# Performance work log

Measured on AMD Instinct MI355X. Metric: run time of the kernel, lower is better.

The kernel has to match this reference:

```python
import jax, jax.numpy as jnp
import numpy as np


def _lstm_layer(x, w_ih, w_hh, b_ih, b_hh):
    # x: [B,T,I]; w_ih: [4H,I]; w_hh: [4H,H]. PyTorch gate order: i,f,g,o.
    B, T, _ = x.shape
    H = w_hh.shape[1]
    xg = jnp.einsum('bti,gi->btg', x, w_ih) + b_ih  # precompute input gates [B,T,4H]

    def step(carry, xt):
        h, c = carry
        g = xt + h @ w_hh.T + b_hh
        i, f, gg, o = jnp.split(g, 4, axis=-1)
        c = jax.nn.sigmoid(f) * c + jax.nn.sigmoid(i) * jnp.tanh(gg)
        h = jax.nn.sigmoid(o) * jnp.tanh(c)
        return (h, c), h

    init = (jnp.zeros((B, H), x.dtype), jnp.zeros((B, H), x.dtype))
    _, hs = jax.lax.scan(step, init, jnp.swapaxes(xg, 0, 1))  # [T,B,H]
    return jnp.swapaxes(hs, 0, 1)


def _lstm2(x, p):  # 2-layer stacked LSTM; p = list of 2 layer param tuples
    for (wih, whh, bih, bhh) in p:
        x = _lstm_layer(x, wih, whh, bih, bhh)
    return x


def setup_inputs() -> dict:
    key = jax.random.key(0)
    ks = iter(jax.random.split(key, 32))
    d = {'x': jax.random.normal(next(ks), (100, 75, 75), jnp.float32)}
    specs = {
        'w_ih_1_0': (512, 75), 'w_hh_1_0': (512, 128), 'b_ih_1_0': (512,), 'b_hh_1_0': (512,),
        'w_ih_1_1': (512, 128), 'w_hh_1_1': (512, 128), 'b_ih_1_1': (512,), 'b_hh_1_1': (512,),
        'w_ih_2_0': (256, 128), 'w_hh_2_0': (256, 64), 'b_ih_2_0': (256,), 'b_hh_2_0': (256,),
        'w_ih_2_1': (256, 64), 'w_hh_2_1': (256, 64), 'b_ih_2_1': (256,), 'b_hh_2_1': (256,),
        'w_ih_3_0': (128, 64), 'w_hh_3_0': (128, 32), 'b_ih_3_0': (128,), 'b_hh_3_0': (128,),
        'w_ih_3_1': (128, 32), 'w_hh_3_1': (128, 32), 'b_ih_3_1': (128,), 'b_hh_3_1': (128,),
        'lin_w': (60, 2400), 'lin_b': (60,),
    }
    for name, shp in specs.items():
        d[name] = jax.random.normal(next(ks), shp, jnp.float32) * 0.1
    return d


def reference(x,
              w_ih_1_0, w_hh_1_0, b_ih_1_0, b_hh_1_0,
              w_ih_1_1, w_hh_1_1, b_ih_1_1, b_hh_1_1,
              w_ih_2_0, w_hh_2_0, b_ih_2_0, b_hh_2_0,
              w_ih_2_1, w_hh_2_1, b_ih_2_1, b_hh_2_1,
              w_ih_3_0, w_hh_3_0, b_ih_3_0, b_hh_3_0,
              w_ih_3_1, w_hh_3_1, b_ih_3_1, b_hh_3_1,
              lin_w, lin_b):
    x = _lstm2(x, [(w_ih_1_0, w_hh_1_0, b_ih_1_0, b_hh_1_0),
                   (w_ih_1_1, w_hh_1_1, b_ih_1_1, b_hh_1_1)])
    x = _lstm2(x, [(w_ih_2_0, w_hh_2_0, b_ih_2_0, b_hh_2_0),
                   (w_ih_2_1, w_hh_2_1, b_ih_2_1, b_hh_2_1)])
    x = _lstm2(x, [(w_ih_3_0, w_hh_3_0, b_ih_3_0, b_hh_3_0),
                   (w_ih_3_1, w_hh_3_1, b_ih_3_1, b_hh_3_1)])
    x = x.reshape((100, 32 * 75))  # [B, T*H] (row-major, matches torch)
    return x @ lin_w.T + lin_b
```

## Files before the change

kernel.cpp:

```cpp
#include <hip/hip_runtime.h>

using half8 = __attribute__((ext_vector_type(8))) _Float16;
using f32x4 = __attribute__((ext_vector_type(4))) float;

__device__ __forceinline__ float sigmf(float x) {
    return __builtin_amdgcn_rcpf(1.0f + __expf(-x));
}
__device__ __forceinline__ float tanhx(float x) {
    return 1.0f - 2.0f * __builtin_amdgcn_rcpf(1.0f + __expf(x + x));
}

struct PrepPtrs {
    const float* wih[6];
    const float* whh[6];
    const float* bi[6];
    const float* bh[6];
    const float* lw;
    _Float16* wihI0;
    _Float16* wihI1;
    _Float16* wihI2;
    _Float16* wihP3;
    _Float16* wihP4;
    _Float16* wihP5;
    _Float16* whhP[6];
    float* biasI;
    float* biasP;
    _Float16* lwI;
};

__global__ __launch_bounds__(256) void prep_kernel(PrepPtrs p) {
    int i = blockIdx.x * 256 + threadIdx.x;
    if (i < 38912) {
        int n = i / 76, k = i - n * 76;
        int col = n >> 2, G = n & 3;
        float v = (k < 75) ? p.wih[0][(size_t)(G * 128 + col) * 75 + k] : 0.0f;
        p.wihI0[i] = (_Float16)v;
        return;
    }
    i -= 38912;
    if (i < 65536) {
        int n = i >> 7, k = i & 127;
        int col = n >> 2, G = n & 3;
        p.wihI1[i] = (_Float16)p.wih[1][(size_t)(G * 128 + col) * 128 + k];
        return;
    }
    i -= 65536;
    if (i < 32768) {
        int n = i >> 7, k = i & 127;
        int col = n >> 2, G = n & 3;
        p.wihI2[i] = (_Float16)p.wih[2][(size_t)(G * 64 + col) * 128 + k];
        return;
    }
    i -= 32768;
    if (i < 16384) { p.wihP3[i] = (_Float16)p.wih[3][i]; return; }
    i -= 16384;
    if (i < 8192) { p.wihP4[i] = (_Float16)p.wih[4][i]; return; }
    i -= 8192;
    if (i < 4096) { p.wihP5[i] = (_Float16)p.wih[5][i]; return; }
    i -= 4096;
    constexpr int WHHC[6] = {65536, 65536, 16384, 16384, 4096, 4096};
    #pragma unroll
    for (int l = 0; l < 6; ++l) {
        if (i < WHHC[l]) { p.whhP[l][i] = (_Float16)p.whh[l][i]; return; }
        i -= WHHC[l];
    }
    if (i < 153600) {
        int t = i >> 11;
        int rem = i & 2047;
        int tile = rem >> 9, op = (rem >> 5) & 15, hc = rem & 31;
        int o = tile * 16 + op;
        float v = (o < 60) ? p.lw[(size_t)o * 2400 + t * 32 + hc] : 0.0f;
        p.lwI[i] = (_Float16)v;
        return;
    }
    i -= 153600;
    constexpr int BIH[3] = {128, 128, 64};
    constexpr int BIO[3] = {0, 512, 1024};
    #pragma unroll
    for (int j = 0; j < 3; ++j) {
        int cnt = 4 * BIH[j];
        if (i < cnt) {
            int col = i >> 2, G = i & 3;
            int src = G * BIH[j] + col;
            p.biasI[BIO[j] + i] = p.bi[j][src] + p.bh[j][src];
            return;
        }
        i -= cnt;
    }
    if (i < 256) { p.biasP[i] = p.bi[3][i] + p.bh[3][i]; return; }
    i -= 256;
    if (i < 128) { p.biasP[256 + i] = p.bi[4][i] + p.bh[4][i]; return; }
    i -= 128;
    if (i < 128) { p.biasP[384 + i] = p.bi[5][i] + p.bh[5][i]; return; }
}

__global__ __launch_bounds__(256) void gemm_xg0(
    const float* __restrict__ X,
    const _Float16* __restrict__ W,
    const float* __restrict__ bias, float* __restrict__ C) {
    constexpr int Ks = 3, KP = 96, LDK = 104, HP = 48, Kv = 76, N = 512;
    __shared__ __align__(16) _Float16 Al[64][LDK];
    __shared__ __align__(16) _Float16 Wl[64][LDK];

    const int tid = threadIdx.x;
    const int tt = blockIdx.x >> 1;
    const int boff = (blockIdx.x & 1) * 48;
    const int n0 = blockIdx.y * 64;

    for (int idx = tid; idx < 64 * HP; idx += 256) {
        int row = idx / HP;
        int k = (idx - row * HP) * 2;
        unsigned int va = 0, vw = 0;
        int b = boff + row;
        if (b < 100 && k < 75) {
            float f0 = X[((size_t)b * 75 + tt) * 75 + k];
            float f1 = (k + 1 < 75) ? X[((size_t)b * 75 + tt) * 75 + k + 1] : 0.0f;
            _Float16 h2[2] = {(_Float16)f0, (_Float16)f1};
            va = *(unsigned int*)h2;
        }
        if (k < Kv) vw = *(const unsigned int*)(W + (size_t)(n0 + row) * Kv + k);
        *(unsigned int*)&Al[row][k] = va;
        *(unsigned int*)&Wl[row][k] = vw;
    }
    __syncthreads();

    const int w = tid >> 6, l = tid & 63, hi = l >> 4;
    half8 a[Ks];
    #pragma unroll
    for (int kk = 0; kk < Ks; ++kk)
        a[kk] = *(const half8*)&Al[w * 16 + (l & 15)][kk * 32 + hi * 8];

    f32x4 acc[4];
    #pragma unroll
    for (int jt = 0; jt < 4; ++jt) {
        acc[jt] = f32x4{0.f, 0.f, 0.f, 0.f};
        #pragma unroll
        for (int kk = 0; kk < Ks; ++kk) {
            half8 b = *(const half8*)&Wl[jt * 16 + (l & 15)][kk * 32 + hi * 8];
            acc[jt] = __builtin_amdgcn_mfma_f32_16x16x32_f16(a[kk], b, acc[jt], 0, 0, 0);
        }
    }

    const int bx = (boff >> 2) + w * 4 + hi;
    #pragma unroll
    for (int jt = 0; jt < 4; ++jt) {
        int n = n0 + jt * 16 + (l & 15);
        float bs = bias[n];
        f32x4 v = acc[jt];
        v[0] += bs; v[1] += bs; v[2] += bs; v[3] += bs;
        *(f32x4*)(C + ((size_t)(tt * 28 + bx) * N + n) * 4) = v;
    }
}

template <int Ks>
__global__ __launch_bounds__(256) void gemm_xg(
    const _Float16* __restrict__ A, const _Float16* __restrict__ W,
    const float* __restrict__ bias, float* __restrict__ C, int Kv, int N) {
    constexpr int KP = Ks * 32;
    constexpr int LDK = KP + 8;
    __shared__ __align__(16) _Float16 Al[64][LDK];
    __shared__ __align__(16) _Float16 Wl[64][LDK];

    const int tid = threadIdx.x;
    const int tt = blockIdx.x >> 1;
    const int boff = (blockIdx.x & 1) * 48;
    const int n0 = blockIdx.y * 64;
    constexpr int HP = KP / 2;

    for (int idx = tid; idx < 64 * HP; idx += 256) {
        int row = idx / HP;
        int k = (idx - row * HP) * 2;
        unsigned int va = 0, vw = 0;
        if (k < Kv) {
            va = *(const unsigned int*)(A + (size_t)(tt * 112 + boff + row) * Kv + k);
            vw = *(const unsigned int*)(W + (size_t)(n0 + row) * Kv + k);
        }
        *(unsigned int*)&Al[row][k] = va;
        *(unsigned int*)&Wl[row][k] = vw;
    }
    __syncthreads();

    const int w = tid >> 6, l = tid & 63, hi = l >> 4;
    half8 a[Ks];
    #pragma unroll
    for (int kk = 0; kk < Ks; ++kk)
        a[kk] = *(const half8*)&Al[w * 16 + (l & 15)][kk * 32 + hi * 8];

    f32x4 acc[4];
    #pragma unroll
    for (int jt = 0; jt < 4; ++jt) {
        acc[jt] = f32x4{0.f, 0.f, 0.f, 0.f};
        #pragma unroll
        for (int kk = 0; kk < Ks; ++kk) {
            half8 b = *(const half8*)&Wl[jt * 16 + (l & 15)][kk * 32 + hi * 8];
            acc[jt] = __builtin_amdgcn_mfma_f32_16x16x32_f16(a[kk], b, acc[jt], 0, 0, 0);
        }
    }

    const int bx = (boff >> 2) + w * 4 + hi;
    #pragma unroll
    for (int jt = 0; jt < 4; ++jt) {
        int n = n0 + jt * 16 + (l & 15);
        float bs = bias[n];
        f32x4 v = acc[jt];
        v[0] += bs; v[1] += bs; v[2] += bs; v[3] += bs;
        *(f32x4*)(C + ((size_t)(tt * 28 + bx) * N + n) * 4) = v;
    }
}

#define FTAIL                                                                 \
    __builtin_amdgcn_sched_barrier(0);                                        \
    asm volatile("s_waitcnt lgkmcnt(0)");                                     \
    __builtin_amdgcn_sched_barrier(0);                                        \
    __builtin_amdgcn_s_barrier();                                             \
    __builtin_amdgcn_sched_barrier(0);

#define PICK(A4) ((hi & 2) ? ((hi & 1) ? A4[3] : A4[2]) : ((hi & 1) ? A4[1] : A4[0]))

#define ACT(aI, aF, aG4, aO)                                                  \
    float gI = PICK(aI), gF = PICK(aF), gG = PICK(aG4), gO = PICK(aO);        \
    float si = sigmf(gI), sf = sigmf(gF), tg = tanhx(gG), so = sigmf(gO);     \
    float cn = sf * cst + si * tg;                                            \
    cst = cn;                                                                 \
    float hn = so * tanhx(cn);                                                \
    _Float16 hv = (_Float16)hn;

template <int H>
__global__ __launch_bounds__(4 * H) void lstm_rec(
    const float* __restrict__ xg, const _Float16* __restrict__ whh,
    _Float16* __restrict__ hout) {
    constexpr int Ks = H / 32;
    constexpr int LDH = H + 8;
    constexpr int XSTR = 448 * H;
    constexpr int HSTR = 112 * H;

    __shared__ __align__(16) _Float16 hbuf[2][4][LDH];

    const int tid = threadIdx.x;
    const int w = tid >> 6, l = tid & 63, hi = l >> 4;
    const int col = w * 16 + (l & 15);
    const int blk = blockIdx.x;

    half8 bw[4][Ks];
    #pragma unroll
    for (int G = 0; G < 4; ++G)
        #pragma unroll
        for (int kk = 0; kk < Ks; ++kk)
            bw[G][kk] = *(const half8*)(whh + (size_t)(G * H + col) * H + kk * 32 + hi * 8);

    for (int i = tid; i < 2 * 4 * LDH; i += 4 * H) ((_Float16*)hbuf)[i] = (_Float16)0;
    __syncthreads();

    const float* xp = xg + (size_t)blk * (4 * H * 4) + col * 16;
    _Float16* hop = hout + (size_t)(blk * 4 + hi) * H + col;

    f32x4 P0[4], P1[4], P2[4];
#define XLOAD(PA)                                                             \
    PA[0] = *(const f32x4*)(xp + 0);                                          \
    PA[1] = *(const f32x4*)(xp + 4);                                          \
    PA[2] = *(const f32x4*)(xp + 8);                                          \
    PA[3] = *(const f32x4*)(xp + 12);                                         \
    xp += XSTR;

    XLOAD(P0)
    XLOAD(P1)
    XLOAD(P2)

    float cst = 0.f;

#define LSTM_STEP(PA, CUR)                                                    \
    {                                                                         \
        half8 afr[Ks];                                                        \
        _Pragma("unroll") for (int kk = 0; kk < Ks; ++kk)                     \
            afr[kk] = *(const half8*)&hbuf[CUR][(l & 15) & 3][kk * 32 + hi * 8]; \
        f32x4 aI = PA[0], aF = PA[1], aG4 = PA[2], aO = PA[3];                \
        XLOAD(PA)                                                             \
        _Pragma("unroll") for (int kk = 0; kk < Ks; ++kk) {                   \
            aI = __builtin_amdgcn_mfma_f32_16x16x32_f16(afr[kk], bw[0][kk], aI, 0, 0, 0);  \
            aF = __builtin_amdgcn_mfma_f32_16x16x32_f16(afr[kk], bw[1][kk], aF, 0, 0, 0);  \
            aG4 = __builtin_amdgcn_mfma_f32_16x16x32_f16(afr[kk], bw[2][kk], aG4, 0, 0, 0);\
            aO = __builtin_amdgcn_mfma_f32_16x16x32_f16(afr[kk], bw[3][kk], aO, 0, 0, 0);  \
        }                                                                     \
        ACT(aI, aF, aG4, aO)                                                  \
        hbuf[CUR ^ 1][hi][col] = hv;                                          \
        *hop = hv;                                                            \
        hop += HSTR;                                                          \
        FTAIL                                                                 \
    }

    #pragma unroll 1
    for (int it = 0; it < 12; ++it) {
        LSTM_STEP(P0, 0) LSTM_STEP(P1, 1) LSTM_STEP(P2, 0)
        LSTM_STEP(P0, 1) LSTM_STEP(P1, 0) LSTM_STEP(P2, 1)
    }
    LSTM_STEP(P0, 0) LSTM_STEP(P1, 1) LSTM_STEP(P2, 0)
#undef LSTM_STEP
#undef XLOAD
}

__global__ __launch_bounds__(832) void lstm_quad(
    const float* __restrict__ xg,
    const _Float16* __restrict__ whh2, const _Float16* __restrict__ whh3,
    const _Float16* __restrict__ wih3, const _Float16* __restrict__ whh4,
    const _Float16* __restrict__ wih4, const _Float16* __restrict__ whh5,
    const _Float16* __restrict__ wih5, const float* __restrict__ biasP,
    const _Float16* __restrict__ lwI,
    const float* __restrict__ lb,
    float* __restrict__ outF) {
    __shared__ __align__(16) _Float16 hb2[2][4][72], hp2[2][4][72];
    __shared__ __align__(16) _Float16 hb3[2][4][72], hp3[2][4][72];
    __shared__ __align__(16) _Float16 hb4[2][4][40], hp4[2][4][40];
    __shared__ __align__(16) _Float16 hb5[2][4][40];

    const int tid = threadIdx.x;
    const int w = tid >> 6, l = tid & 63, hi = l >> 4;
    const int lr = (l & 15) & 3;
    const int blk = blockIdx.x;

    for (int i = tid; i < 2 * 4 * 72; i += 832) {
        ((_Float16*)hb2)[i] = (_Float16)0; ((_Float16*)hp2)[i] = (_Float16)0;
        ((_Float16*)hb3)[i] = (_Float16)0; ((_Float16*)hp3)[i] = (_Float16)0;
    }
    for (int i = tid; i < 2 * 4 * 40; i += 832) {
        ((_Float16*)hb4)[i] = (_Float16)0; ((_Float16*)hp4)[i] = (_Float16)0;
        ((_Float16*)hb5)[i] = (_Float16)0;
    }
    __syncthreads();

    float cst = 0.f;

    if (w < 4) {
        const int col = w * 16 + (l & 15);
        half8 bw[4][2];
        #pragma unroll
        for (int G = 0; G < 4; ++G)
            #pragma unroll
            for (int kk = 0; kk < 2; ++kk)
                bw[G][kk] = *(const half8*)(whh2 + (size_t)(G * 64 + col) * 64 + kk * 32 + hi * 8);
        const float* xp = xg + (size_t)blk * 1024 + col * 16;
        f32x4 P0[4], P1[4], P2[4];
#define XLOADQ(PA)                                                            \
        PA[0] = *(const f32x4*)(xp + 0);                                      \
        PA[1] = *(const f32x4*)(xp + 4);                                      \
        PA[2] = *(const f32x4*)(xp + 8);                                      \
        PA[3] = *(const f32x4*)(xp + 12);                                     \
        xp += 28672;
        XLOADQ(P0)
        XLOADQ(P1)
        XLOADQ(P2)

#define QA(PA, CUR, S)                                                        \
        {                                                                     \
            if ((S) < 75) {                                                   \
                half8 afr[2];                                                 \
                _Pragma("unroll") for (int kk = 0; kk < 2; ++kk)              \
                    afr[kk] = *(const half8*)&hb2[CUR][lr][kk * 32 + hi * 8]; \
                f32x4 aI = PA[0], aF = PA[1], aG4 = PA[2], aO = PA[3];        \
                XLOADQ(PA)                                                    \
                _Pragma("unroll") for (int kk = 0; kk < 2; ++kk) {            \
                    aI = __builtin_amdgcn_mfma_f32_16x16x32_f16(afr[kk], bw[0][kk], aI, 0, 0, 0);  \
                    aF = __builtin_amdgcn_mfma_f32_16x16x32_f16(afr[kk], bw[1][kk], aF, 0, 0, 0);  \
                    aG4 = __builtin_amdgcn_mfma_f32_16x16x32_f16(afr[kk], bw[2][kk], aG4, 0, 0, 0);\
                    aO = __builtin_amdgcn_mfma_f32_16x16x32_f16(afr[kk], bw[3][kk], aO, 0, 0, 0);  \
                }                                                             \
                ACT(aI, aF, aG4, aO)                                          \
                hb2[(CUR) ^ 1][hi][col] = hv;                                 \
                hp2[(CUR) ^ 1][hi][col] = hv;                                 \
            }                                                                 \
            FTAIL                                                             \
        }
        #pragma unroll 1
        for (int it = 0; it < 13; ++it) {
            const int b6 = it * 6;
            QA(P0, 0, b6 + 0) QA(P1, 1, b6 + 1) QA(P2, 0, b6 + 2)
            QA(P0, 1, b6 + 3) QA(P1, 0, b6 + 4) QA(P2, 1, b6 + 5)
        }
#undef QA
#undef XLOADQ
    } else if (w < 8) {
        const int col = (w - 4) * 16 + (l & 15);
        half8 bwB[4][2], bwI[4][2];
        #pragma unroll
        for (int G = 0; G < 4; ++G)
            #pragma unroll
            for (int kk = 0; kk < 2; ++kk) {
                bwB[G][kk] = *(const half8*)(whh3 + (size_t)(G * 64 + col) * 64 + kk * 32 + hi * 8);
                bwI[G][kk] = *(const half8*)(wih3 + (size_t)(G * 64 + col) * 64 + kk * 32 + hi * 8);
            }
        const float bI = biasP[col], bF = biasP[64 + col];
        const float bG = biasP[128 + col], bO = biasP[192 + col];
        #pragma unroll 1
        for (int s = 0; s < 78; ++s) {
            const int cur = s & 1;
            if (s >= 1 && s <= 75) {
                half8 afr[2], air[2];
                #pragma unroll
                for (int kk = 0; kk < 2; ++kk) {
                    afr[kk] = *(const half8*)&hb3[cur][lr][kk * 32 + hi * 8];
                    air[kk] = *(const half8*)&hp2[cur][lr][kk * 32 + hi * 8];
                }
                f32x4 aI = {bI, bI, bI, bI}, aF = {bF, bF, bF, bF};
                f32x4 aG4 = {bG, bG, bG, bG}, aO = {bO, bO, bO, bO};
                #pragma unroll
                for (int kk = 0; kk < 2; ++kk) {
                    aI = __builtin_amdgcn_mfma_f32_16x16x32_f16(afr[kk], bwB[0][kk], aI, 0, 0, 0);
                    aF = __builtin_amdgcn_mfma_f32_16x16x32_f16(afr[kk], bwB[1][kk], aF, 0, 0, 0);
                    aG4 = __builtin_amdgcn_mfma_f32_16x16x32_f16(afr[kk], bwB[2][kk], aG4, 0, 0, 0);
                    aO = __builtin_amdgcn_mfma_f32_16x16x32_f16(afr[kk], bwB[3][kk], aO, 0, 0, 0);
                }
                #pragma unroll
                for (int kk = 0; kk < 2; ++kk) {
                    aI = __builtin_amdgcn_mfma_f32_16x16x32_f16(air[kk], bwI[0][kk], aI, 0, 0, 0);
                    aF = __builtin_amdgcn_mfma_f32_16x16x32_f16(air[kk], bwI[1][kk], aF, 0, 0, 0);
                    aG4 = __builtin_amdgcn_mfma_f32_16x16x32_f16(air[kk], bwI[2][kk], aG4, 0, 0, 0);
                    aO = __builtin_amdgcn_mfma_f32_16x16x32_f16(air[kk], bwI[3][kk], aO, 0, 0, 0);
                }
                ACT(aI, aF, aG4, aO)
                hb3[cur ^ 1][hi][col] = hv;
                hp3[cur ^ 1][hi][col] = hv;
            }
            FTAIL
        }
    } else if (w < 10) {
        const int col = (w - 8) * 16 + (l & 15);
        half8 bwB[4], bwI[4][2];
        #pragma unroll
        for (int G = 0; G < 4; ++G) {
            bwB[G] = *(const half8*)(whh4 + (size_t)(G * 32 + col) * 32 + hi * 8);
            #pragma unroll
            for (int kk = 0; kk < 2; ++kk)
                bwI[G][kk] = *(const half8*)(wih4 + (size_t)(G * 32 + col) * 64 + kk * 32 + hi * 8);
        }
        const float* bp = biasP + 256;
        const float bI = bp[col], bF = bp[32 + col], bG = bp[64 + col], bO = bp[96 + col];
        #pragma unroll 1
        for (int s = 0; s < 78; ++s) {
            const int cur = s & 1;
            if (s >= 2 && s <= 76) {
                half8 afr = *(const half8*)&hb4[cur][lr][hi * 8];
                half8 air[2];
                #pragma unroll
                for (int kk = 0; kk < 2; ++kk)
                    air[kk] = *(const half8*)&hp3[cur][lr][kk * 32 + hi * 8];
                f32x4 aI = {bI, bI, bI, bI}, aF = {bF, bF, bF, bF};
                f32x4 aG4 = {bG, bG, bG, bG}, aO = {bO, bO, bO, bO};
                aI = __builtin_amdgcn_mfma_f32_16x16x32_f16(afr, bwB[0], aI, 0, 0, 0);
                aF = __builtin_amdgcn_mfma_f32_16x16x32_f16(afr, bwB[1], aF, 0, 0, 0);
                aG4 = __builtin_amdgcn_mfma_f32_16x16x32_f16(afr, bwB[2], aG4, 0, 0, 0);
                aO = __builtin_amdgcn_mfma_f32_16x16x32_f16(afr, bwB[3], aO, 0, 0, 0);
                #pragma unroll
                for (int kk = 0; kk < 2; ++kk) {
                    aI = __builtin_amdgcn_mfma_f32_16x16x32_f16(air[kk], bwI[0][kk], aI, 0, 0, 0);
                    aF = __builtin_amdgcn_mfma_f32_16x16x32_f16(air[kk], bwI[1][kk], aF, 0, 0, 0);
                    aG4 = __builtin_amdgcn_mfma_f32_16x16x32_f16(air[kk], bwI[2][kk], aG4, 0, 0, 0);
                    aO = __builtin_amdgcn_mfma_f32_16x16x32_f16(air[kk], bwI[3][kk], aO, 0, 0, 0);
                }
                ACT(aI, aF, aG4, aO)
                hb4[cur ^ 1][hi][col] = hv;
                hp4[cur ^ 1][hi][col] = hv;
            }
            FTAIL
        }
    } else if (w < 12) {
        const int col = (w - 10) * 16 + (l & 15);
        half8 bwB[4], bwI[4];
        #pragma unroll
        for (int G = 0; G < 4; ++G) {
            bwB[G] = *(const half8*)(whh5 + (size_t)(G * 32 + col) * 32 + hi * 8);
            bwI[G] = *(const half8*)(wih5 + (size_t)(G * 32 + col) * 32 + hi * 8);
        }
        const float* bp = biasP + 384;
        const float bI = bp[col], bF = bp[32 + col], bG = bp[64 + col], bO = bp[96 + col];
        #pragma unroll 1
        for (int s = 0; s < 78; ++s) {
            const int cur = s & 1;
            if (s >= 3) {
                half8 afr = *(const half8*)&hb5[cur][lr][hi * 8];
                half8 air = *(const half8*)&hp4[cur][lr][hi * 8];
                f32x4 aI = {bI, bI, bI, bI}, aF = {bF, bF, bF, bF};
                f32x4 aG4 = {bG, bG, bG, bG}, aO = {bO, bO, bO, bO};
                aI = __builtin_amdgcn_mfma_f32_16x16x32_f16(afr, bwB[0], aI, 0, 0, 0);
                aF = __builtin_amdgcn_mfma_f32_16x16x32_f16(afr, bwB[1], aF, 0, 0, 0);
                aG4 = __builtin_amdgcn_mfma_f32_16x16x32_f16(afr, bwB[2], aG4, 0, 0, 0);
                aO = __builtin_amdgcn_mfma_f32_16x16x32_f16(afr, bwB[3], aO, 0, 0, 0);
                aI = __builtin_amdgcn_mfma_f32_16x16x32_f16(air, bwI[0], aI, 0, 0, 0);
                aF = __builtin_amdgcn_mfma_f32_16x16x32_f16(air, bwI[1], aF, 0, 0, 0);
                aG4 = __builtin_amdgcn_mfma_f32_16x16x32_f16(air, bwI[2], aG4, 0, 0, 0);
                aO = __builtin_amdgcn_mfma_f32_16x16x32_f16(air, bwI[3], aO, 0, 0, 0);
                ACT(aI, aF, aG4, aO)
                hb5[cur ^ 1][hi][col] = hv;
            }
            FTAIL
        }
    } else {
        const int ln = l & 15;
        const _Float16* lwp = lwI + (size_t)ln * 32 + hi * 8;
        half8 LA[4], LB[4];
        #pragma unroll
        for (int tl = 0; tl < 4; ++tl) {
            LA[tl] = *(const half8*)(lwp + (size_t)(0 * 4 + tl) * 512);
            LB[tl] = *(const half8*)(lwp + (size_t)(1 * 4 + tl) * 512);
        }
        f32x4 acc[4];
        #pragma unroll
        for (int tl = 0; tl < 4; ++tl) acc[tl] = f32x4{0.f, 0.f, 0.f, 0.f};

        #pragma unroll 1
        for (int it = 0; it < 39; ++it) {
            {
                int t = 2 * it - 4;
                if (t >= 0) {
                    half8 hf = *(const half8*)&hb5[0][lr][hi * 8];
                    #pragma unroll
                    for (int tl = 0; tl < 4; ++tl)
                        acc[tl] = __builtin_amdgcn_mfma_f32_16x16x32_f16(LA[tl], hf, acc[tl], 0, 0, 0);
                }
                int tn = t + 2;
                if (tn < 0) tn = 0;
                if (tn > 74) tn = 74;
                #pragma unroll
                for (int tl = 0; tl < 4; ++tl)
                    LA[tl] = *(const half8*)(lwp + ((size_t)tn * 4 + tl) * 512);
                FTAIL
            }
            {
                int t = 2 * it - 3;
                if (t >= 0) {
                    half8 hf = *(const half8*)&hb5[1][lr][hi * 8];
                    #pragma unroll
                    for (int tl = 0; tl < 4; ++tl)
                        acc[tl] = __builtin_amdgcn_mfma_f32_16x16x32_f16(LB[tl], hf, acc[tl], 0, 0, 0);
                }
                int tn = t + 2;
                if (tn < 0) tn = 0;
                if (tn > 74) tn = 74;
                #pragma unroll
                for (int tl = 0; tl < 4; ++tl)
                    LB[tl] = *(const half8*)(lwp + ((size_t)tn * 4 + tl) * 512);
                FTAIL
            }
        }
        {
            half8 hf = *(const half8*)&hb5[0][lr][hi * 8];
            #pragma unroll
            for (int tl = 0; tl < 4; ++tl)
                acc[tl] = __builtin_amdgcn_mfma_f32_16x16x32_f16(LA[tl], hf, acc[tl], 0, 0, 0);
        }
        if (ln < 4) {
            int b = blk * 4 + ln;
            #pragma unroll
            for (int tl = 0; tl < 4; ++tl)
                #pragma unroll
                for (int r = 0; r < 4; ++r) {
                    int o = tl * 16 + hi * 4 + r;
                    if (o < 60) outF[b * 60 + o] = acc[tl][r] + lb[o];
                }
        }
    }
}

extern "C" void kernel_launch(void* const* d_in, const int* in_sizes, int n_in,
                              void* d_out, int out_size, void* d_ws, size_t ws_size,
                              hipStream_t stream) {
    const float* x = (const float*)d_in[0];
    const float* wih[6];
    const float* whhp[6];
    const float* bih[6];
    const float* bhh[6];
    for (int i = 0; i < 6; ++i) {
        wih[i] = (const float*)d_in[1 + 4 * i];
        whhp[i] = (const float*)d_in[2 + 4 * i];
        bih[i] = (const float*)d_in[3 + 4 * i];
        bhh[i] = (const float*)d_in[4 + 4 * i];
    }
    const float* lw = (const float*)d_in[25];
    const float* lb = (const float*)d_in[26];
    float* out = (float*)d_out;

    char* ws = (char*)d_ws;
    size_t cur = 0;
    auto alloc = [&](size_t b) {
        size_t o = cur;
        cur += (b + 255) & ~(size_t)255;
        return o;
    };
    _Float16* wihI0 = (_Float16*)(ws + alloc(38912 * 2));
    _Float16* wihI1 = (_Float16*)(ws + alloc(65536 * 2));
    _Float16* wihI2 = (_Float16*)(ws + alloc(32768 * 2));
    _Float16* wihP3 = (_Float16*)(ws + alloc(16384 * 2));
    _Float16* wihP4 = (_Float16*)(ws + alloc(8192 * 2));
    _Float16* wihP5 = (_Float16*)(ws + alloc(4096 * 2));
    _Float16* whhP[6];
    const size_t whhBytes[6] = {131072, 131072, 32768, 32768, 8192, 8192};
    for (int i = 0; i < 6; ++i) whhP[i] = (_Float16*)(ws + alloc(whhBytes[i]));
    _Float16* lwI = (_Float16*)(ws + alloc(153600 * 2));
    float* biasI = (float*)(ws + alloc(1280 * 4));
    float* biasP = (float*)(ws + alloc(512 * 4));
    float* xg = (float*)(ws + alloc((size_t)78 * 28 * 512 * 4 * 4));
    _Float16* h0 = (_Float16*)(ws + alloc((size_t)75 * 112 * 128 * 2));
    _Float16* h1 = (_Float16*)(ws + alloc((size_t)75 * 112 * 128 * 2));

    PrepPtrs pp;
    for (int i = 0; i < 6; ++i) {
        pp.wih[i] = wih[i];
        pp.whh[i] = whhp[i];
        pp.bi[i] = bih[i];
        pp.bh[i] = bhh[i];
        pp.whhP[i] = whhP[i];
    }
    pp.lw = lw;
    pp.wihI0 = wihI0;
    pp.wihI1 = wihI1;
    pp.wihI2 = wihI2;
    pp.wihP3 = wihP3;
    pp.wihP4 = wihP4;
    pp.wihP5 = wihP5;
    pp.biasI = biasI;
    pp.biasP = biasP;
    pp.lwI = lwI;
    prep_kernel<<<1927, 256, 0, stream>>>(pp);

    gemm_xg0<<<dim3(150, 8), 256, 0, stream>>>(x, wihI0, biasI + 0, xg);
    lstm_rec<128><<<25, 512, 0, stream>>>(xg, whhP[0], h0);
    gemm_xg<4><<<dim3(150, 8), 256, 0, stream>>>(h0, wihI1, biasI + 512, xg, 128, 512);
    lstm_rec<128><<<25, 512, 0, stream>>>(xg, whhP[1], h1);
    gemm_xg<4><<<dim3(150, 4), 256, 0, stream>>>(h1, wihI2, biasI + 1024, xg, 128, 256);
    lstm_quad<<<25, 832, 0, stream>>>(xg, whhP[2], whhP[3], wihP3, whhP[4],
                                      wihP4, whhP[5], wihP5, biasP, lwI, lb, out);
}
```

Measured before the change: 180.4 us.

## Fold weight prep into consumers and fuse layer-2 input GEMM into layer-1 recurrence

Removes the big prep kernel, which converted and permuted all weights and biases to fp16. Each kernel now converts fp32 weights and sums biases itself when loading them. The layer-1 recurrence kernel gets extra waves that compute layer-2's input-gate projection from the freshly produced hidden states, one step behind. This drops the separate gemm_xg launch and the h1 round trip through memory. In exchange there is redundant fp32 loading and conversion per block, wider LDS padding, and a 768-thread block whose extra waves join every step barrier.

```diff
diff --git a/kernel.cpp b/kernel.cpp
--- a/kernel.cpp
+++ b/kernel.cpp
@@ -9,96 +9,35 @@
 __device__ __forceinline__ float tanhx(float x) {
     return 1.0f - 2.0f * __builtin_amdgcn_rcpf(1.0f + __expf(x + x));
 }
-
-struct PrepPtrs {
-    const float* wih[6];
-    const float* whh[6];
-    const float* bi[6];
-    const float* bh[6];
-    const float* lw;
-    _Float16* wihI0;
-    _Float16* wihI1;
-    _Float16* wihI2;
-    _Float16* wihP3;
-    _Float16* wihP4;
-    _Float16* wihP5;
-    _Float16* whhP[6];
-    float* biasI;
-    float* biasP;
-    _Float16* lwI;
-};
-
-__global__ __launch_bounds__(256) void prep_kernel(PrepPtrs p) {
+__device__ __forceinline__ half8 cvt8(const float* p) {
+    f32x4 a = *(const f32x4*)p;
+    f32x4 b = *(const f32x4*)(p + 4);
+    half8 r;
+    r[0] = (_Float16)a[0]; r[1] = (_Float16)a[1];
+    r[2] = (_Float16)a[2]; r[3] = (_Float16)a[3];
+    r[4] = (_Float16)b[0]; r[5] = (_Float16)b[1];
+    r[6] = (_Float16)b[2]; r[7] = (_Float16)b[3];
+    return r;
+}
+
+__global__ __launch_bounds__(256) void prep_lw(const float* __restrict__ lw,
+                                               _Float16* __restrict__ lwI) {
     int i = blockIdx.x * 256 + threadIdx.x;
-    if (i < 38912) {
-        int n = i / 76, k = i - n * 76;
-        int col = n >> 2, G = n & 3;
-        float v = (k < 75) ? p.wih[0][(size_t)(G * 128 + col) * 75 + k] : 0.0f;
-        p.wihI0[i] = (_Float16)v;
-        return;
-    }
-    i -= 38912;
-    if (i < 65536) {
-        int n = i >> 7, k = i & 127;
-        int col = n >> 2, G = n & 3;
-        p.wihI1[i] = (_Float16)p.wih[1][(size_t)(G * 128 + col) * 128 + k];
-        return;
-    }
-    i -= 65536;
-    if (i < 32768) {
-        int n = i >> 7, k = i & 127;
-        int col = n >> 2, G = n & 3;
-        p.wihI2[i] = (_Float16)p.wih[2][(size_t)(G * 64 + col) * 128 + k];
-        return;
-    }
-    i -= 32768;
-    if (i < 16384) { p.wihP3[i] = (_Float16)p.wih[3][i]; return; }
-    i -= 16384;
-    if (i < 8192) { p.wihP4[i] = (_Float16)p.wih[4][i]; return; }
-    i -= 8192;
-    if (i < 4096) { p.wihP5[i] = (_Float16)p.wih[5][i]; return; }
-    i -= 4096;
-    constexpr int WHHC[6] = {65536, 65536, 16384, 16384, 4096, 4096};
-    #pragma unroll
-    for (int l = 0; l < 6; ++l) {
-        if (i < WHHC[l]) { p.whhP[l][i] = (_Float16)p.whh[l][i]; return; }
-        i -= WHHC[l];
-    }
-    if (i < 153600) {
-        int t = i >> 11;
-        int rem = i & 2047;
-        int tile = rem >> 9, op = (rem >> 5) & 15, hc = rem & 31;
-        int o = tile * 16 + op;
-        float v = (o < 60) ? p.lw[(size_t)o * 2400 + t * 32 + hc] : 0.0f;
-        p.lwI[i] = (_Float16)v;
-        return;
-    }
-    i -= 153600;
-    constexpr int BIH[3] = {128, 128, 64};
-    constexpr int BIO[3] = {0, 512, 1024};
-    #pragma unroll
-    for (int j = 0; j < 3; ++j) {
-        int cnt = 4 * BIH[j];
-        if (i < cnt) {
-            int col = i >> 2, G = i & 3;
-            int src = G * BIH[j] + col;
-            p.biasI[BIO[j] + i] = p.bi[j][src] + p.bh[j][src];
-            return;
-        }
-        i -= cnt;
-    }
-    if (i < 256) { p.biasP[i] = p.bi[3][i] + p.bh[3][i]; return; }
-    i -= 256;
-    if (i < 128) { p.biasP[256 + i] = p.bi[4][i] + p.bh[4][i]; return; }
-    i -= 128;
-    if (i < 128) { p.biasP[384 + i] = p.bi[5][i] + p.bh[5][i]; return; }
+    if (i >= 153600) return;
+    int t = i >> 11;
+    int rem = i & 2047;
+    int tile = rem >> 9, op = (rem >> 5) & 15, hc = rem & 31;
+    int o = tile * 16 + op;
+    float v = (o < 60) ? lw[(size_t)o * 2400 + t * 32 + hc] : 0.0f;
+    lwI[i] = (_Float16)v;
 }
 
 __global__ __launch_bounds__(256) void gemm_xg0(
     const float* __restrict__ X,
-    const _Float16* __restrict__ W,
-    const float* __restrict__ bias, float* __restrict__ C) {
-    constexpr int Ks = 3, KP = 96, LDK = 104, HP = 48, Kv = 76, N = 512;
+    const float* __restrict__ W0,
+    const float* __restrict__ bi0, const float* __restrict__ bh0,
+    float* __restrict__ C) {
+    constexpr int Ks = 3, LDK = 104, HP = 48, N = 512;
     __shared__ __align__(16) _Float16 Al[64][LDK];
     __shared__ __align__(16) _Float16 Wl[64][LDK];
 
@@ -118,7 +57,14 @@
             _Float16 h2[2] = {(_Float16)f0, (_Float16)f1};
             va = *(unsigned int*)h2;
         }
-        if (k < Kv) vw = *(const unsigned int*)(W + (size_t)(n0 + row) * Kv + k);
+        if (k < 75) {
+            int n = n0 + row;
+            int src = (n & 3) * 128 + (n >> 2);
+            float f0 = W0[(size_t)src * 75 + k];
+            float f1 = (k + 1 < 75) ? W0[(size_t)src * 75 + k + 1] : 0.0f;
+            _Float16 h2[2] = {(_Float16)f0, (_Float16)f1};
+            vw = *(unsigned int*)h2;
+        }
         *(unsigned int*)&Al[row][k] = va;
         *(unsigned int*)&Wl[row][k] = vw;
     }
@@ -145,19 +91,20 @@
     #pragma unroll
     for (int jt = 0; jt < 4; ++jt) {
         int n = n0 + jt * 16 + (l & 15);
-        float bs = bias[n];
+        int src = (n & 3) * 128 + (n >> 2);
+        float bs = bi0[src] + bh0[src];
         f32x4 v = acc[jt];
         v[0] += bs; v[1] += bs; v[2] += bs; v[3] += bs;
         *(f32x4*)(C + ((size_t)(tt * 28 + bx) * N + n) * 4) = v;
     }
 }
 
-template <int Ks>
-__global__ __launch_bounds__(256) void gemm_xg(
-    const _Float16* __restrict__ A, const _Float16* __restrict__ W,
-    const float* __restrict__ bias, float* __restrict__ C, int Kv, int N) {
-    constexpr int KP = Ks * 32;
-    constexpr int LDK = KP + 8;
+__global__ __launch_bounds__(256) void gemm_xg1(
+    const _Float16* __restrict__ A,
+    const float* __restrict__ W1,
+    const float* __restrict__ bi1, const float* __restrict__ bh1,
+    float* __restrict__ C) {
+    constexpr int Ks = 4, LDK = 136, HP = 64, Kv = 128, N = 512;
     __shared__ __align__(16) _Float16 Al[64][LDK];
     __shared__ __align__(16) _Float16 Wl[64][LDK];
 
@@ -165,18 +112,18 @@
     const int tt = blockIdx.x >> 1;
     const int boff = (blockIdx.x & 1) * 48;
     const int n0 = blockIdx.y * 64;
-    constexpr int HP = KP / 2;
 
     for (int idx = tid; idx < 64 * HP; idx += 256) {
         int row = idx / HP;
         int k = (idx - row * HP) * 2;
-        unsigned int va = 0, vw = 0;
-        if (k < Kv) {
-            va = *(const unsigned int*)(A + (size_t)(tt * 112 + boff + row) * Kv + k);
-            vw = *(const unsigned int*)(W + (size_t)(n0 + row) * Kv + k);
-        }
+        unsigned int va = *(const unsigned int*)(A + (size_t)(tt * 112 + boff + row) * Kv + k);
+        int n = n0 + row;
+        int src = (n & 3) * 128 + (n >> 2);
+        float f0 = W1[(size_t)src * 128 + k];
+        float f1 = W1[(size_t)src * 128 + k + 1];
+        _Float16 h2[2] = {(_Float16)f0, (_Float16)f1};
         *(unsigned int*)&Al[row][k] = va;
-        *(unsigned int*)&Wl[row][k] = vw;
+        *(unsigned int*)&Wl[row][k] = *(unsigned int*)h2;
     }
     __syncthreads();
 
@@ -201,7 +148,8 @@
     #pragma unroll
     for (int jt = 0; jt < 4; ++jt) {
         int n = n0 + jt * 16 + (l & 15);
-        float bs = bias[n];
+        int src = (n & 3) * 128 + (n >> 2);
+        float bs = bi1[src] + bh1[src];
         f32x4 v = acc[jt];
         v[0] += bs; v[1] += bs; v[2] += bs; v[3] += bs;
         *(f32x4*)(C + ((size_t)(tt * 28 + bx) * N + n) * 4) = v;
@@ -225,12 +173,11 @@
     float hn = so * tanhx(cn);                                                \
     _Float16 hv = (_Float16)hn;
 
-template <int H>
-__global__ __launch_bounds__(4 * H) void lstm_rec(
-    const float* __restrict__ xg, const _Float16* __restrict__ whh,
+__global__ __launch_bounds__(512) void lstm_rec0(
+    const float* __restrict__ xg,
+    const float* __restrict__ whhf,
     _Float16* __restrict__ hout) {
-    constexpr int Ks = H / 32;
-    constexpr int LDH = H + 8;
+    constexpr int H = 128, Ks = 4, LDH = 160;
     constexpr int XSTR = 448 * H;
     constexpr int HSTR = 112 * H;
 
@@ -246,9 +193,9 @@
     for (int G = 0; G < 4; ++G)
         #pragma unroll
         for (int kk = 0; kk < Ks; ++kk)
-            bw[G][kk] = *(const half8*)(whh + (size_t)(G * H + col) * H + kk * 32 + hi * 8);
-
-    for (int i = tid; i < 2 * 4 * LDH; i += 4 * H) ((_Float16*)hbuf)[i] = (_Float16)0;
+            bw[G][kk] = cvt8(whhf + (size_t)(G * H + col) * H + kk * 32 + hi * 8);
+
+    for (int i = tid; i < 2 * 4 * LDH; i += 512) ((_Float16*)hbuf)[i] = (_Float16)0;
     __syncthreads();
 
     const float* xp = xg + (size_t)blk * (4 * H * 4) + col * 16;
@@ -298,30 +245,152 @@
 #undef XLOAD
 }
 
-__global__ __launch_bounds__(832) void lstm_quad(
-    const float* __restrict__ xg,
-    const _Float16* __restrict__ whh2, const _Float16* __restrict__ whh3,
-    const _Float16* __restrict__ wih3, const _Float16* __restrict__ whh4,
-    const _Float16* __restrict__ wih4, const _Float16* __restrict__ whh5,
-    const _Float16* __restrict__ wih5, const float* __restrict__ biasP,
-    const _Float16* __restrict__ lwI,
-    const float* __restrict__ lb,
-    float* __restrict__ outF) {
-    __shared__ __align__(16) _Float16 hb2[2][4][72], hp2[2][4][72];
-    __shared__ __align__(16) _Float16 hb3[2][4][72], hp3[2][4][72];
-    __shared__ __align__(16) _Float16 hb4[2][4][40], hp4[2][4][40];
-    __shared__ __align__(16) _Float16 hb5[2][4][40];
+__global__ __launch_bounds__(768) void rec1xg(
+    const float* __restrict__ xg1,
+    const float* __restrict__ whh1f,
+    const float* __restrict__ wih2f,
+    const float* __restrict__ bi2, const float* __restrict__ bh2,
+    float* __restrict__ xg2) {
+    constexpr int H = 128, Ks = 4, LDH = 160;
+    constexpr int XSTR = 448 * H;
+
+    __shared__ __align__(16) _Float16 hb1[2][4][LDH];
+    __shared__ __align__(16) _Float16 hp[2][4][LDH];
 
     const int tid = threadIdx.x;
     const int w = tid >> 6, l = tid & 63, hi = l >> 4;
     const int lr = (l & 15) & 3;
     const int blk = blockIdx.x;
 
-    for (int i = tid; i < 2 * 4 * 72; i += 832) {
+    for (int i = tid; i < 2 * 4 * LDH; i += 768) {
+        ((_Float16*)hb1)[i] = (_Float16)0;
+        ((_Float16*)hp)[i] = (_Float16)0;
+    }
+    __syncthreads();
+
+    float cst = 0.f;
+
+    if (w < 8) {
+        const int col = w * 16 + (l & 15);
+        half8 bw[4][Ks];
+        #pragma unroll
+        for (int G = 0; G < 4; ++G)
+            #pragma unroll
+            for (int kk = 0; kk < Ks; ++kk)
+                bw[G][kk] = cvt8(whh1f + (size_t)(G * H + col) * H + kk * 32 + hi * 8);
+
+        const float* xp = xg1 + (size_t)blk * (4 * H * 4) + col * 16;
+        f32x4 P0[4], P1[4];
+#define XLOADA(PA)                                                            \
+        PA[0] = *(const f32x4*)(xp + 0);                                      \
+        PA[1] = *(const f32x4*)(xp + 4);                                      \
+        PA[2] = *(const f32x4*)(xp + 8);                                      \
+        PA[3] = *(const f32x4*)(xp + 12);                                     \
+        xp += XSTR;
+        XLOADA(P0)
+        XLOADA(P1)
+
+#define ASTEP(PA, CUR)                                                        \
+        {                                                                     \
+            half8 afr[Ks];                                                    \
+            _Pragma("unroll") for (int kk = 0; kk < Ks; ++kk)                 \
+                afr[kk] = *(const half8*)&hb1[CUR][lr][kk * 32 + hi * 8];     \
+            f32x4 aI = PA[0], aF = PA[1], aG4 = PA[2], aO = PA[3];            \
+            XLOADA(PA)                                                        \
+            _Pragma("unroll") for (int kk = 0; kk < Ks; ++kk) {               \
+                aI = __builtin_amdgcn_mfma_f32_16x16x32_f16(afr[kk], bw[0][kk], aI, 0, 0, 0);  \
+                aF = __builtin_amdgcn_mfma_f32_16x16x32_f16(afr[kk], bw[1][kk], aF, 0, 0, 0);  \
+                aG4 = __builtin_amdgcn_mfma_f32_16x16x32_f16(afr[kk], bw[2][kk], aG4, 0, 0, 0);\
+                aO = __builtin_amdgcn_mfma_f32_16x16x32_f16(afr[kk], bw[3][kk], aO, 0, 0, 0);  \
+            }                                                                 \
+            ACT(aI, aF, aG4, aO)                                              \
+            hb1[(CUR) ^ 1][hi][col] = hv;                                     \
+            hp[(CUR) ^ 1][hi][col] = hv;                                      \
+        }
+
+        #pragma unroll 1
+        for (int it = 0; it < 38; ++it) {
+            ASTEP(P0, 0)
+            FTAIL
+            if (2 * it + 1 < 75) { ASTEP(P1, 1) }
+            FTAIL
+        }
+#undef ASTEP
+#undef XLOADA
+    } else {
+        const int col = (w - 8) * 16 + (l & 15);
+        half8 bwI[4][Ks];
+        #pragma unroll
+        for (int G = 0; G < 4; ++G)
+            #pragma unroll
+            for (int kk = 0; kk < Ks; ++kk)
+                bwI[G][kk] = cvt8(wih2f + (size_t)(G * 64 + col) * 128 + kk * 32 + hi * 8);
+        float bb[4];
+        #pragma unroll
+        for (int G = 0; G < 4; ++G) bb[G] = bi2[G * 64 + col] + bh2[G * 64 + col];
+        float* xq = xg2 + (size_t)blk * 1024 + col * 16;
+
+        #pragma unroll 1
+        for (int s = 0; s < 76; ++s) {
+            const int cur = s & 1;
+            if (s >= 1) {
+                half8 air[Ks];
+                #pragma unroll
+                for (int kk = 0; kk < Ks; ++kk)
+                    air[kk] = *(const half8*)&hp[cur][lr][kk * 32 + hi * 8];
+                f32x4 acc[4];
+                #pragma unroll
+                for (int G = 0; G < 4; ++G)
+                    acc[G] = f32x4{bb[G], bb[G], bb[G], bb[G]};
+                #pragma unroll
+                for (int G = 0; G < 4; ++G)
+                    #pragma unroll
+                    for (int kk = 0; kk < Ks; ++kk)
+                        acc[G] = __builtin_amdgcn_mfma_f32_16x16x32_f16(air[kk], bwI[G][kk], acc[G], 0, 0, 0);
+                if (hi == 0) {
+                    #pragma unroll
+                    for (int G = 0; G < 4; ++G)
+                        *(f32x4*)(xq + (size_t)(s - 1) * 28672 + G * 4) = acc[G];
+                }
+            }
+            FTAIL
+        }
+    }
+}
+
+struct QuadPtrs {
+    const float* xg;
+    const float* whh2;
+    const float* whh3;
+    const float* wih3;
+    const float* whh4;
+    const float* wih4;
+    const float* whh5;
+    const float* wih5;
+    const float* bi3; const float* bh3;
+    const float* bi4; const float* bh4;
+    const float* bi5; const float* bh5;
+    const _Float16* lwI;
+    const float* lb;
+    float* outF;
+};
+
+__global__ __launch_bounds__(832) void lstm_quad(QuadPtrs q) {
+    __shared__ __align__(16) _Float16 hb2[2][4][96], hp2[2][4][96];
+    __shared__ __align__(16) _Float16 hb3[2][4][96], hp3[2][4][96];
+    __shared__ __align__(16) _Float16 hb4[2][4][80], hp4[2][4][80];
+    __shared__ __align__(16) _Float16 hb5[2][4][80];
+
+    const int tid = threadIdx.x;
+    const int w = tid >> 6, l = tid & 63, hi = l >> 4;
+    const int lr = (l & 15) & 3;
+    const int blk = blockIdx.x;
+
+    for (int i = tid; i < 2 * 4 * 96; i += 832) {
         ((_Float16*)hb2)[i] = (_Float16)0; ((_Float16*)hp2)[i] = (_Float16)0;
         ((_Float16*)hb3)[i] = (_Float16)0; ((_Float16*)hp3)[i] = (_Float16)0;
     }
-    for (int i = tid; i < 2 * 4 * 40; i += 832) {
+    for (int i = tid; i < 2 * 4 * 80; i += 832) {
         ((_Float16*)hb4)[i] = (_Float16)0; ((_Float16*)hp4)[i] = (_Float16)0;
         ((_Float16*)hb5)[i] = (_Float16)0;
     }
@@ -336,8 +405,8 @@
         for (int G = 0; G < 4; ++G)
             #pragma unroll
             for (int kk = 0; kk < 2; ++kk)
-                bw[G][kk] = *(const half8*)(whh2 + (size_t)(G * 64 + col) * 64 + kk * 32 + hi * 8);
-        const float* xp = xg + (size_t)blk * 1024 + col * 16;
+                bw[G][kk] = cvt8(q.whh2 + (size_t)(G * 64 + col) * 64 + kk * 32 + hi * 8);
+        const float* xp = q.xg + (size_t)blk * 1024 + col * 16;
         f32x4 P0[4], P1[4], P2[4];
 #define XLOADQ(PA)                                                            \
         PA[0] = *(const f32x4*)(xp + 0);                                      \
@@ -384,11 +453,13 @@
         for (int G = 0; G < 4; ++G)
             #pragma unroll
             for (int kk = 0; kk < 2; ++kk) {
-                bwB[G][kk] = *(const half8*)(whh3 + (size_t)(G * 64 + col) * 64 + kk * 32 + hi * 8);
-                bwI[G][kk] = *(const half8*)(wih3 + (size_t)(G * 64 + col) * 64 + kk * 32 + hi * 8);
+                bwB[G][kk] = cvt8(q.whh3 + (size_t)(G * 64 + col) * 64 + kk * 32 + hi * 8);
+                bwI[G][kk] = cvt8(q.wih3 + (size_t)(G * 64 + col) * 64 + kk * 32 + hi * 8);
             }
-        const float bI = biasP[col], bF = biasP[64 + col];
-        const float bG = biasP[128 + col], bO = biasP[192 + col];
+        const float bI = q.bi3[col] + q.bh3[col];
+        const float bF = q.bi3[64 + col] + q.bh3[64 + col];
+        const float bG = q.bi3[128 + col] + q.bh3[128 + col];
+        const float bO = q.bi3[192 + col] + q.bh3[192 + col];
         #pragma unroll 1
         for (int s = 0; s < 78; ++s) {
             const int cur = s & 1;
@@ -426,13 +497,15 @@
         half8 bwB[4], bwI[4][2];
         #pragma unroll
         for (int G = 0; G < 4; ++G) {
-            bwB[G] = *(const half8*)(whh4 + (size_t)(G * 32 + col) * 32 + hi * 8);
+            bwB[G] = cvt8(q.whh4 + (size_t)(G * 32 + col) * 32 + hi * 8);
             #pragma unroll
             for (int kk = 0; kk < 2; ++kk)
-                bwI[G][kk] = *(const half8*)(wih4 + (size_t)(G * 32 + col) * 64 + kk * 32 + hi * 8);
-        }
-        const float* bp = biasP + 256;
-        const float bI = bp[col], bF = bp[32 + col], bG = bp[64 + col], bO = bp[96 + col];
+                bwI[G][kk] = cvt8(q.wih4 + (size_t)(G * 32 + col) * 64 + kk * 32 + hi * 8);
+        }
+        const float bI = q.bi4[col] + q.bh4[col];
+        const float bF = q.bi4[32 + col] + q.bh4[32 + col];
+        const float bG = q.bi4[64 + col] + q.bh4[64 + col];
+        const float bO = q.bi4[96 + col] + q.bh4[96 + col];
         #pragma unroll 1
         for (int s = 0; s < 78; ++s) {
             const int cur = s & 1;
@@ -466,11 +539,13 @@
         half8 bwB[4], bwI[4];
         #pragma unroll
         for (int G = 0; G < 4; ++G) {
-            bwB[G] = *(const half8*)(whh5 + (size_t)(G * 32 + col) * 32 + hi * 8);
-            bwI[G] = *(const half8*)(wih5 + (size_t)(G * 32 + col) * 32 + hi * 8);
-        }
-        const float* bp = biasP + 384;
-        const float bI = bp[col], bF = bp[32 + col], bG = bp[64 + col], bO = bp[96 + col];
+            bwB[G] = cvt8(q.whh5 + (size_t)(G * 32 + col) * 32 + hi * 8);
+            bwI[G] = cvt8(q.wih5 + (size_t)(G * 32 + col) * 32 + hi * 8);
+        }
+        const float bI = q.bi5[col] + q.bh5[col];
+        const float bF = q.bi5[32 + col] + q.bh5[32 + col];
+        const float bG = q.bi5[64 + col] + q.bh5[64 + col];
+        const float bO = q.bi5[96 + col] + q.bh5[96 + col];
         #pragma unroll 1
         for (int s = 0; s < 78; ++s) {
             const int cur = s & 1;
@@ -494,7 +569,7 @@
         }
     } else {
         const int ln = l & 15;
-        const _Float16* lwp = lwI + (size_t)ln * 32 + hi * 8;
+        const _Float16* lwp = q.lwI + (size_t)ln * 32 + hi * 8;
         half8 LA[4], LB[4];
         #pragma unroll
         for (int tl = 0; tl < 4; ++tl) {
@@ -553,7 +628,7 @@
                 #pragma unroll
                 for (int r = 0; r < 4; ++r) {
                     int o = tl * 16 + hi * 4 + r;
-                    if (o < 60) outF[b * 60 + o] = acc[tl][r] + lb[o];
+                    if (o < 60) q.outF[b * 60 + o] = acc[tl][r] + q.lb[o];
                 }
         }
     }
@@ -584,47 +659,24 @@
         cur += (b + 255) & ~(size_t)255;
         return o;
     };
-    _Float16* wihI0 = (_Float16*)(ws + alloc(38912 * 2));
-    _Float16* wihI1 = (_Float16*)(ws + alloc(65536 * 2));
-    _Float16* wihI2 = (_Float16*)(ws + alloc(32768 * 2));
-    _Float16* wihP3 = (_Float16*)(ws + alloc(16384 * 2));
-    _Float16* wihP4 = (_Float16*)(ws + alloc(8192 * 2));
-    _Float16* wihP5 = (_Float16*)(ws + alloc(4096 * 2));
-    _Float16* whhP[6];
-    const size_t whhBytes[6] = {131072, 131072, 32768, 32768, 8192, 8192};
-    for (int i = 0; i < 6; ++i) whhP[i] = (_Float16*)(ws + alloc(whhBytes[i]));
     _Float16* lwI = (_Float16*)(ws + alloc(153600 * 2));
-    float* biasI = (float*)(ws + alloc(1280 * 4));
-    float* biasP = (float*)(ws + alloc(512 * 4));
-    float* xg = (float*)(ws + alloc((size_t)78 * 28 * 512 * 4 * 4));
+    float* xgA = (float*)(ws + alloc((size_t)78 * 28 * 512 * 4 * 4));
+    float* xgB = (float*)(ws + alloc((size_t)78 * 28 * 256 * 4 * 4));
     _Float16* h0 = (_Float16*)(ws + alloc((size_t)75 * 112 * 128 * 2));
-    _Float16* h1 = (_Float16*)(ws + alloc((size_t)75 * 112 * 128 * 2));
-
-    PrepPtrs pp;
-    for (int i = 0; i < 6; ++i) {
-        pp.wih[i] = wih[i];
-        pp.whh[i] = whhp[i];
-        pp.bi[i] = bih[i];
-        pp.bh[i] = bhh[i];
-        pp.whhP[i] = whhP[i];
-    }
-    pp.lw = lw;
-    pp.wihI0 = wihI0;
-    pp.wihI1 = wihI1;
-    pp.wihI2 = wihI2;
-    pp.wihP3 = wihP3;
-    pp.wihP4 = wihP4;
-    pp.wihP5 = wihP5;
-    pp.biasI = biasI;
-    pp.biasP = biasP;
-    pp.lwI = lwI;
-    prep_kernel<<<1927, 256, 0, stream>>>(pp);
-
-    gemm_xg0<<<dim3(150, 8), 256, 0, stream>>>(x, wihI0, biasI + 0, xg);
-    lstm_rec<128><<<25, 512, 0, stream>>>(xg, whhP[0], h0);
-    gemm_xg<4><<<dim3(150, 8), 256, 0, stream>>>(h0, wihI1, biasI + 512, xg, 128, 512);
-    lstm_rec<128><<<25, 512, 0, stream>>>(xg, whhP[1], h1);
-    gemm_xg<4><<<dim3(150, 4), 256, 0, stream>>>(h1, wihI2, biasI + 1024, xg, 128, 256);
-    lstm_quad<<<25, 832, 0, stream>>>(xg, whhP[2], whhP[3], wihP3, whhP[4],
-                                      wihP4, whhP[5], wihP5, biasP, lwI, lb, out);
-}
+
+    prep_lw<<<600, 256, 0, stream>>>(lw, lwI);
+
+    gemm_xg0<<<dim3(150, 8), 256, 0, stream>>>(x, wih[0], bih[0], bhh[0], xgA);
+    lstm_rec0<<<25, 512, 0, stream>>>(xgA, whhp[0], h0);
+    gemm_xg1<<<dim3(150, 8), 256, 0, stream>>>(h0, wih[1], bih[1], bhh[1], xgA);
+    rec1xg<<<25, 768, 0, stream>>>(xgA, whhp[1], wih[2], bih[2], bhh[2], xgB);
+    QuadPtrs q;
+    q.xg = xgB;
+    q.whh2 = whhp[2]; q.whh3 = whhp[3]; q.wih3 = wih[3];
+    q.whh4 = whhp[4]; q.wih4 = wih[4]; q.whh5 = whhp[5]; q.wih5 = wih[5];
+    q.bi3 = bih[3]; q.bh3 = bhh[3];
+    q.bi4 = bih[4]; q.bh4 = bhh[4];
+    q.bi5 = bih[5]; q.bh5 = bhh[5];
+    q.lwI = lwI; q.lb = lb; q.outF = out;
+    lstm_quad<<<25, 832, 0, stream>>>(q);
+}
```

Result: slower. 212.0 us (+17.5%).
